# Kernel optimization log

Hardware: AMD Instinct MI355X
Metric: run time of the kernel (lower is better)

Reference implementation:

```python
import jax, jax.numpy as jnp
import numpy as np
from jax import lax


def _conv3x3(x, w, b):
    # x: [b,C,H,W], w: [Cout,Cin,3,3] (OIHW), same padding, stride 1
    y = lax.conv_general_dilated(
        x, w, window_strides=(1, 1), padding='SAME',
        dimension_numbers=('NCHW', 'OIHW', 'NCHW'))
    return y + b[None, :, None, None]


def setup_inputs() -> dict:
    key = jax.random.key(0)
    ks = jax.random.split(key, 8)
    b, C, H, W = 8, 256, 64, 64
    wscale = 0.02  # keep conv outputs O(1) so softmax logits are well-conditioned
    X = jax.random.normal(ks[0], (b, C, H, W), dtype=jnp.float32)
    w1 = jax.random.normal(ks[1], (C, C, 3, 3), dtype=jnp.float32) * wscale
    b1 = jax.random.normal(ks[2], (C,), dtype=jnp.float32) * 0.01
    w2 = jax.random.normal(ks[3], (C, C, 3, 3), dtype=jnp.float32) * wscale
    b2 = jax.random.normal(ks[4], (C,), dtype=jnp.float32) * 0.01
    w3 = jax.random.normal(ks[5], (C, C, 3, 3), dtype=jnp.float32) * wscale
    b3 = jax.random.normal(ks[6], (C,), dtype=jnp.float32) * 0.01
    # alpha_init=0 in the original makes the output identically zero; use a
    # small nonzero alpha so fwd/bwd are non-degenerate for correctness checks.
    alpha = jax.random.normal(ks[7], (), dtype=jnp.float32)
    return {"X": X, "w1": w1, "b1": b1, "w2": w2, "b2": b2,
            "w3": w3, "b3": b3, "alpha": alpha}


def reference(X, w1, b1, w2, b2, w3, b3, alpha):
    b, C, H, W = X.shape
    N = H * W
    A = _conv3x3(X, w1, b1).reshape(b, C, N)  # [b,C,N]
    B = _conv3x3(X, w2, b2).reshape(b, C, N)  # [b,C,N]
    D = _conv3x3(X, w3, b3).reshape(b, C, N)  # [b,C,N]
    # M = softmax(A^T B) over last dim; M: [b,N,N]
    M = jnp.einsum('bcn,bcm->bnm', A, B)
    M = jax.nn.softmax(M, axis=-1)
    # weighted_C = M @ D^T -> [b,N,C]; then to [b,C,H,W]
    out = jnp.einsum('bnm,bcm->bcn', M, D).reshape(b, C, H, W)
    return alpha * out
```

## Files before the change

kernel.cpp:

```cpp
#include <hip/hip_runtime.h>
#include <math.h>

#define BATCH 8
#define CCH   256
#define HH    64
#define WW    64
#define NN    4096

#define BNC   (BATCH * NN * CCH)
#define WELEMS (3 * 8 * 9 * 256 * 32)

typedef __bf16   bf16x8 __attribute__((ext_vector_type(8)));
typedef _Float16 f16x8  __attribute__((ext_vector_type(8)));
typedef _Float16 f16x4  __attribute__((ext_vector_type(4)));
typedef float    f32x4  __attribute__((ext_vector_type(4)));

__global__ void wtrans_kernel(const float* __restrict__ w1,
                              const float* __restrict__ w2,
                              const float* __restrict__ w3,
                              _Float16* __restrict__ Whi,
                              _Float16* __restrict__ Wlo) {
    int e = blockIdx.x * 256 + threadIdx.x;
    int t = e;
    const int ci  = t & 31;  t >>= 5;
    const int co  = t & 255; t >>= 8;
    const int tap = t % 9;   t /= 9;
    const int cc  = t & 7;   t >>= 3;
    const int conv = t;
    const float* src = (conv == 0) ? w1 : (conv == 1) ? w2 : w3;
    const float v = src[co * 2304 + (cc * 32 + ci) * 9 + tap];
    const _Float16 h = (_Float16)v;
    Whi[e] = h;
    Wlo[e] = (_Float16)(v - (float)h);
}

__global__ __launch_bounds__(256)
void xsplit_kernel(const float* __restrict__ X,
                   _Float16* __restrict__ Xhi, _Float16* __restrict__ Xlo) {
    __shared__ float T[64][65];
    const int h = blockIdx.x, c0 = blockIdx.y * 64, bb = blockIdx.z;
    const int t = threadIdx.x;
    const int row = t >> 2, q = (t & 3) * 16;
#pragma unroll
    for (int k = 0; k < 4; ++k) {
        float4 v = *(const float4*)&X[(((size_t)bb * CCH + c0 + row) * HH + h) * WW + q + k * 4];
        *(float4*)&T[row][q + k * 4] = v;
    }
    __syncthreads();
    f16x8 h0, h1, l0, l1;
#pragma unroll
    for (int j = 0; j < 8; ++j) {
        float v = T[q + j][row];
        _Float16 hh = (_Float16)v;
        h0[j] = hh; l0[j] = (_Float16)(v - (float)hh);
    }
#pragma unroll
    for (int j = 0; j < 8; ++j) {
        float v = T[q + 8 + j][row];
        _Float16 hh = (_Float16)v;
        h1[j] = hh; l1[j] = (_Float16)(v - (float)hh);
    }
    const size_t g = (((size_t)bb * HH + h) * WW + row) * CCH + c0 + q;
    *(f16x8*)(Xhi + g) = h0;  *(f16x8*)(Xhi + g + 8) = h1;
    *(f16x8*)(Xlo + g) = l0;  *(f16x8*)(Xlo + g + 8) = l1;
}

__global__ __launch_bounds__(512, 2)
void conv_mfma_kernel(const _Float16* __restrict__ Xhi, const _Float16* __restrict__ Xlo,
                      const _Float16* __restrict__ Whi, const _Float16* __restrict__ Wlo,
                      const float* __restrict__ b1, const float* __restrict__ b2,
                      const float* __restrict__ b3,
                      __bf16* __restrict__ Qhi, __bf16* __restrict__ Qlo,
                      __bf16* __restrict__ Khi, __bf16* __restrict__ Klo,
                      float* __restrict__ Dws) {
    const int h0   = blockIdx.x * 2;
    const int bb   = blockIdx.y;
    const int conv = blockIdx.z;
    const int tid  = threadIdx.x;
    const int wave = tid >> 6;
    const int lane = tid & 63;
    const int quad = lane >> 4;
    const int l16  = lane & 15;
    const int mg   = wave >> 2;
    const int ng   = wave & 3;

    __shared__ _Float16 XsH[4 * 66 * 32];
    __shared__ _Float16 XsL[4 * 66 * 32];

    const bool threePass = (conv < 2);
    const float* bias = (conv == 0) ? b1 : (conv == 1) ? b2 : b3;

    f32x4 acc[4][4];
#pragma unroll
    for (int j = 0; j < 4; ++j) {
        const float bv = bias[ng * 64 + j * 16 + l16];
#pragma unroll
        for (int i = 0; i < 4; ++i) acc[i][j] = (f32x4){bv, bv, bv, bv};
    }

    const f16x8 zf = {0, 0, 0, 0, 0, 0, 0, 0};
    const int xrow = tid >> 7;
    const int xw   = (tid >> 1) & 63;
    const int xch  = (tid & 1) * 16;
    const int xc0  = (tid & 1) * 2;

    if (tid < 256) {
        const int zr = tid >> 6, zc = ((tid >> 5) & 1) ? 65 : 0, zch = tid & 31;
        XsH[(zr * 66 + zc) * 32 + zch] = (_Float16)0;
        XsL[(zr * 66 + zc) * 32 + zch] = (_Float16)0;
    }

    int xb[3];
#pragma unroll
    for (int dw = 0; dw < 3; ++dw)
        xb[dw] = mg * 2112 + (l16 + dw) * 32 + ((quad ^ ((l16 + dw) & 3)) * 8);

    const int wloff = (ng * 64 + l16) * 32 + quad * 8;
    const _Float16* WhB = Whi + (size_t)conv * 589824;
    const _Float16* WlB = Wlo + (size_t)conv * 589824;

    f16x8 wbh[2][4], wbl[2][4];
#pragma unroll
    for (int j = 0; j < 4; ++j) {
        wbh[0][j] = *(const f16x8*)(WhB + wloff + j * 512);
        wbl[0][j] = zf;
        if (threePass) wbl[0][j] = *(const f16x8*)(WlB + wloff + j * 512);
    }

    for (int cc2 = 0; cc2 < 4; ++cc2) {
#pragma unroll
        for (int ccp = 0; ccp < 2; ++ccp) {
            const int cc = cc2 * 2 + ccp;
            __syncthreads();
            {
                const int h = h0 - 1 + xrow;
                f16x8 a0 = zf, a1 = zf, b0 = zf, b1v = zf;
                if ((unsigned)h < (unsigned)HH) {
                    const size_t g = (((size_t)bb * HH + h) * WW + xw) * CCH + cc * 32 + xch;
                    a0 = *(const f16x8*)(Xhi + g);  a1 = *(const f16x8*)(Xhi + g + 8);
                    if (threePass) { b0 = *(const f16x8*)(Xlo + g);  b1v = *(const f16x8*)(Xlo + g + 8); }
                }
                const int col = xw + 1;
                const int lbase = (xrow * 66 + col) * 32;
                const int s3 = col & 3;
                *(f16x8*)&XsH[lbase + ((xc0 ^ s3) * 8)]       = a0;
                *(f16x8*)&XsH[lbase + (((xc0 + 1) ^ s3) * 8)] = a1;
                if (threePass) {
                    *(f16x8*)&XsL[lbase + ((xc0 ^ s3) * 8)]       = b0;
                    *(f16x8*)&XsL[lbase + (((xc0 + 1) ^ s3) * 8)] = b1v;
                }
            }
            __syncthreads();

#pragma unroll
            for (int tap = 0; tap < 9; ++tap) {
                const int p  = (ccp + tap) & 1;
                const int np = p ^ 1;
                {
                    const int nst = cc * 9 + tap + 1;
                    const size_t nb = (size_t)(nst == 72 ? 0 : nst) * 8192 + wloff;
#pragma unroll
                    for (int j = 0; j < 4; ++j) {
                        wbh[np][j] = *(const f16x8*)(WhB + nb + j * 512);
                        if (threePass) wbl[np][j] = *(const f16x8*)(WlB + nb + j * 512);
                    }
                }
                const int dh = tap / 3, dw = tap % 3;
                f16x8 ah[4], al[4];
#pragma unroll
                for (int i = 0; i < 4; ++i) {
                    const int off = xb[dw] + dh * 2112 + i * 512;
                    ah[i] = *(const f16x8*)&XsH[off];
                    if (threePass) al[i] = *(const f16x8*)&XsL[off];
                }
#pragma unroll
                for (int j = 0; j < 4; ++j) {
                    if (threePass) {
#pragma unroll
                        for (int i = 0; i < 4; ++i) {
                            acc[i][j] = __builtin_amdgcn_mfma_f32_16x16x32_f16(ah[i], wbh[p][j], acc[i][j], 0, 0, 0);
                            acc[i][j] = __builtin_amdgcn_mfma_f32_16x16x32_f16(al[i], wbh[p][j], acc[i][j], 0, 0, 0);
                            acc[i][j] = __builtin_amdgcn_mfma_f32_16x16x32_f16(ah[i], wbl[p][j], acc[i][j], 0, 0, 0);
                        }
                    } else {
#pragma unroll
                        for (int i = 0; i < 4; ++i)
                            acc[i][j] = __builtin_amdgcn_mfma_f32_16x16x32_f16(ah[i], wbh[p][j], acc[i][j], 0, 0, 0);
                    }
                }
            }
        }
    }

    const size_t nb = (size_t)bb * NN + (size_t)(h0 + mg) * 64;
    if (threePass) {
        __bf16* Hi = conv ? Khi : Qhi;
        __bf16* Lo = conv ? Klo : Qlo;
#pragma unroll
        for (int i = 0; i < 4; ++i) {
            const int wx0 = i * 16 + quad * 4;
#pragma unroll
            for (int j = 0; j < 4; ++j) {
                const int co = ng * 64 + j * 16 + l16;
#pragma unroll
                for (int r = 0; r < 4; ++r) {
                    const float v = acc[i][j][r];
                    const size_t idx = (nb + wx0 + r) * CCH + co;
                    const __bf16 hq = (__bf16)v;
                    Hi[idx] = hq;
                    Lo[idx] = (__bf16)(v - (float)hq);
                }
            }
        }
    } else {
#pragma unroll
        for (int i = 0; i < 4; ++i) {
            const int wx0 = i * 16 + quad * 4;
#pragma unroll
            for (int j = 0; j < 4; ++j) {
                const int co = ng * 64 + j * 16 + l16;
#pragma unroll
                for (int r = 0; r < 4; ++r)
                    Dws[(nb + wx0 + r) * CCH + co] = acc[i][j][r];
            }
        }
    }
}

__global__ __launch_bounds__(256)
void transpose_v_kernel(const float* __restrict__ D, _Float16* __restrict__ Vt) {
    __shared__ float T[64][65];
    const int n0 = blockIdx.x * 64, c0 = blockIdx.y * 64, bb = blockIdx.z;
    const int t = threadIdx.x;
    const int row = t >> 2, q = (t & 3) * 16;
#pragma unroll
    for (int k = 0; k < 4; ++k) {
        float4 v = *(const float4*)(D + ((size_t)bb * NN + n0 + row) * CCH + c0 + q + k * 4);
        *(float4*)&T[row][q + k * 4] = v;
    }
    __syncthreads();
    f16x8 o0, o1;
#pragma unroll
    for (int j = 0; j < 8; ++j) o0[j] = (_Float16)T[q + j][row];
#pragma unroll
    for (int j = 0; j < 8; ++j) o1[j] = (_Float16)T[q + 8 + j][row];
    _Float16* dst = Vt + ((size_t)bb * CCH + c0 + row) * NN + n0 + q;
    *(f16x8*)dst = o0;
    *(f16x8*)(dst + 8) = o1;
}

__global__ __launch_bounds__(512, 2)
void attn_mfma_kernel(const __bf16* __restrict__ Qhi, const __bf16* __restrict__ Qlo,
                      const __bf16* __restrict__ Khi, const __bf16* __restrict__ Klo,
                      const _Float16* __restrict__ Vt, const float* __restrict__ alpha_p,
                      float* __restrict__ out) {
    const int bb = blockIdx.x & 7;
    const int qb = blockIdx.x >> 3;
    const int n0 = qb * 128;
    const int tid  = threadIdx.x;
    const int wave = tid >> 6;
    const int lane = tid & 63;
    const int quad = lane >> 4;
    const int l16  = lane & 15;
    const int xq   = l16 & 7;

    extern __shared__ __align__(16) unsigned char smem[];
    __bf16*   KsHi = (__bf16*)(smem);
    __bf16*   KsLo = (__bf16*)(smem + 16384);
    _Float16* Vs   = (_Float16*)(smem + 32768);
    _Float16* Pw   = (_Float16*)(smem + 98304) + wave * 16 * 136;

    bf16x8 qh[8], ql[8];
    {
        const size_t base = ((size_t)bb * NN + n0 + wave * 16 + l16) * CCH + quad * 8;
#pragma unroll
        for (int ks = 0; ks < 8; ++ks) {
            qh[ks] = *(const bf16x8*)(Qhi + base + ks * 32);
            ql[ks] = *(const bf16x8*)(Qlo + base + ks * 32);
        }
    }

    f32x4 Oacc[16];
#pragma unroll
    for (int cf = 0; cf < 16; ++cf) Oacc[cf] = (f32x4){0.f, 0.f, 0.f, 0.f};
    float m_i = -INFINITY, l_i = 0.f;

    const int krow = tid >> 2, kq4 = tid & 3;
    const int vrow = tid >> 1, vh = tid & 1;

    bf16x8 kph[2], kpl[2];
    f16x8  vp[4];

    auto kload = [&](int m0_, int cc_) {
#pragma unroll
        for (int i = 0; i < 2; ++i) {
            const int u = kq4 * 2 + i;
            const size_t g = ((size_t)bb * NN + m0_ + krow) * CCH + cc_ * 64 + u * 8;
            kph[i] = *(const bf16x8*)(Khi + g);
            kpl[i] = *(const bf16x8*)(Klo + g);
        }
    };
    auto kwrite = [&]() {
#pragma unroll
        for (int i = 0; i < 2; ++i) {
            const int u = kq4 * 2 + i;
            const int lo = krow * 64 + ((u ^ (krow & 7)) * 8);
            *(bf16x8*)&KsHi[lo] = kph[i];
            *(bf16x8*)&KsLo[lo] = kpl[i];
        }
    };
    auto vload = [&](int m0_, int grp) {
#pragma unroll
        for (int i = 0; i < 4; ++i) {
            const int u = grp * 8 + vh * 4 + i;
            vp[i] = *(const f16x8*)(Vt + ((size_t)bb * CCH + vrow) * NN + m0_ + u * 8);
        }
    };
    auto vwrite = [&](int grp) {
#pragma unroll
        for (int i = 0; i < 4; ++i) {
            const int u = grp * 8 + vh * 4 + i;
            *(f16x8*)&Vs[vrow * 128 + ((u ^ (vrow & 7)) * 8)] = vp[i];
        }
    };

    f32x4 Sacc[8];
    auto schunk = [&](int cc) {
#pragma unroll
        for (int ks = 0; ks < 2; ++ks) {
            const int kq = cc * 2 + ks;
#pragma unroll
            for (int kvt = 0; kvt < 8; ++kvt) {
                const int off = (kvt * 16 + l16) * 64 + (((ks * 4 + quad) ^ xq) * 8);
                const bf16x8 kh = *(const bf16x8*)&KsHi[off];
                const bf16x8 kl = *(const bf16x8*)&KsLo[off];
                Sacc[kvt] = __builtin_amdgcn_mfma_f32_16x16x32_bf16(kh, qh[kq], Sacc[kvt], 0, 0, 0);
                Sacc[kvt] = __builtin_amdgcn_mfma_f32_16x16x32_bf16(kl, qh[kq], Sacc[kvt], 0, 0, 0);
                Sacc[kvt] = __builtin_amdgcn_mfma_f32_16x16x32_bf16(kh, ql[kq], Sacc[kvt], 0, 0, 0);
            }
        }
    };

    kload(0, 0);
    kwrite();
    __syncthreads();

    for (int t = 0; t < 32; ++t) {
        const int m0 = t * 128;
#pragma unroll
        for (int kvt = 0; kvt < 8; ++kvt) Sacc[kvt] = (f32x4){0.f, 0.f, 0.f, 0.f};

        for (int cc = 0; cc < 3; ++cc) {
            kload(m0, cc + 1);
            schunk(cc);
            __syncthreads();
            kwrite();
            __syncthreads();
        }

        vload(m0, 0);
        schunk(3);
        vwrite(0);
        vload(m0, 1);

        float mx = -INFINITY;
#pragma unroll
        for (int kvt = 0; kvt < 8; ++kvt)
#pragma unroll
            for (int r = 0; r < 4; ++r) mx = fmaxf(mx, Sacc[kvt][r]);
        mx = fmaxf(mx, __shfl_xor(mx, 16, 64));
        mx = fmaxf(mx, __shfl_xor(mx, 32, 64));
        const float mnew = fmaxf(m_i, mx);
        float rs = 0.f;
#pragma unroll
        for (int kvt = 0; kvt < 8; ++kvt) {
            f16x4 pw;
#pragma unroll
            for (int r = 0; r < 4; ++r) {
                const float p = __expf(Sacc[kvt][r] - mnew);
                rs += p;
                pw[r] = (_Float16)p;
            }
            *(f16x4*)&Pw[l16 * 136 + kvt * 16 + quad * 4] = pw;
        }
        rs += __shfl_xor(rs, 16, 64);
        rs += __shfl_xor(rs, 32, 64);
        const float scale = __expf(m_i - mnew);
        l_i = l_i * scale + rs;
        m_i = mnew;
#pragma unroll
        for (int cf = 0; cf < 16; ++cf) {
            Oacc[cf][0] *= scale;
            Oacc[cf][1] *= scale;
            Oacc[cf][2] *= scale;
            Oacc[cf][3] *= scale;
        }
        vwrite(1);
        __syncthreads();

        kload((t == 31) ? 0 : m0 + 128, 0);
        f16x8 pf[4];
#pragma unroll
        for (int kvf = 0; kvf < 4; ++kvf)
            pf[kvf] = *(const f16x8*)&Pw[l16 * 136 + kvf * 32 + quad * 8];
#pragma unroll
        for (int cf = 0; cf < 16; ++cf) {
#pragma unroll
            for (int kvf = 0; kvf < 4; ++kvf) {
                const f16x8 vf = *(const f16x8*)&Vs[(cf * 16 + l16) * 128 + (((kvf * 4 + quad) ^ xq) * 8)];
                Oacc[cf] = __builtin_amdgcn_mfma_f32_16x16x32_f16(vf, pf[kvf], Oacc[cf], 0, 0, 0);
            }
        }
        kwrite();
        __syncthreads();
    }

    const float alpha = *alpha_p;
    const float inv = alpha / l_i;
    const int qg = n0 + wave * 16 + l16;
#pragma unroll
    for (int cf = 0; cf < 16; ++cf) {
#pragma unroll
        for (int r = 0; r < 4; ++r) {
            const int c = cf * 16 + quad * 4 + r;
            out[((size_t)bb * CCH + c) * NN + qg] = Oacc[cf][r] * inv;
        }
    }
}

extern "C" void kernel_launch(void* const* d_in, const int* in_sizes, int n_in,
                              void* d_out, int out_size, void* d_ws, size_t ws_size,
                              hipStream_t stream) {
    const float* X  = (const float*)d_in[0];
    const float* w1 = (const float*)d_in[1];
    const float* b1 = (const float*)d_in[2];
    const float* w2 = (const float*)d_in[3];
    const float* b2 = (const float*)d_in[4];
    const float* w3 = (const float*)d_in[5];
    const float* b3 = (const float*)d_in[6];
    const float* alpha = (const float*)d_in[7];
    float* out = (float*)d_out;

    float*    Dws = (float*)d_ws;
    __bf16*   Qhi = (__bf16*)(Dws + (size_t)BNC);
    __bf16*   Qlo = Qhi + (size_t)BNC;
    __bf16*   Khi = Qlo + (size_t)BNC;
    __bf16*   Klo = Khi + (size_t)BNC;
    _Float16* Vt  = (_Float16*)(Klo + (size_t)BNC);
    _Float16* Xhi = Vt + (size_t)BNC;
    _Float16* Xlo = Xhi + (size_t)BNC;
    _Float16* Whi = Xlo + (size_t)BNC;
    _Float16* Wlo = Whi + (size_t)WELEMS;

    wtrans_kernel<<<dim3(WELEMS / 256), 256, 0, stream>>>(w1, w2, w3, Whi, Wlo);

    xsplit_kernel<<<dim3(HH, CCH / 64, BATCH), 256, 0, stream>>>(X, Xhi, Xlo);

    conv_mfma_kernel<<<dim3(HH / 2, BATCH, 3), 512, 0, stream>>>(
        Xhi, Xlo, Whi, Wlo, b1, b2, b3, Qhi, Qlo, Khi, Klo, Dws);

    transpose_v_kernel<<<dim3(NN / 64, CCH / 64, BATCH), 256, 0, stream>>>(Dws, Vt);

    attn_mfma_kernel<<<dim3(256), 512, 133120, stream>>>(
        Qhi, Qlo, Khi, Klo, Vt, alpha, out);
}
```

Measured before the change: 586.2 us.

## Split PV GEMM by channel per wave, loading V directly into registers

The PV product is repartitioned. Each wave now owns 32 output channels for all 128 queries instead of 16 queries for all 256 channels, and reads its V fragments straight from global memory into registers instead of staging V through shared memory. K staging becomes double-buffered, so each chunk needs one barrier instead of two. P tiles and the per-row rescale factors and final normalisers are shared through LDS, which shrinks the LDS footprint. The cost is uncoalesced-ish direct global V loads, extra LDS reads of P for all query tiles, and a different output store pattern.

```diff
diff --git a/kernel.cpp b/kernel.cpp
--- a/kernel.cpp
+++ b/kernel.cpp
@@ -265,10 +265,10 @@
     const int xq   = l16 & 7;
 
     extern __shared__ __align__(16) unsigned char smem[];
-    __bf16*   KsHi = (__bf16*)(smem);
-    __bf16*   KsLo = (__bf16*)(smem + 16384);
-    _Float16* Vs   = (_Float16*)(smem + 32768);
-    _Float16* Pw   = (_Float16*)(smem + 98304) + wave * 16 * 136;
+    _Float16* PwA  = (_Float16*)(smem + 65536);
+    float*    Ssc  = (float*)(smem + 100352);
+    float*    Linv = (float*)(smem + 100864);
+    _Float16* Pw   = PwA + wave * (16 * 136);
 
     bf16x8 qh[8], ql[8];
     {
@@ -280,16 +280,16 @@
         }
     }
 
-    f32x4 Oacc[16];
-#pragma unroll
-    for (int cf = 0; cf < 16; ++cf) Oacc[cf] = (f32x4){0.f, 0.f, 0.f, 0.f};
+    f32x4 Oacc[2][8];
+#pragma unroll
+    for (int cf = 0; cf < 2; ++cf)
+#pragma unroll
+        for (int qt = 0; qt < 8; ++qt) Oacc[cf][qt] = (f32x4){0.f, 0.f, 0.f, 0.f};
     float m_i = -INFINITY, l_i = 0.f;
 
     const int krow = tid >> 2, kq4 = tid & 3;
-    const int vrow = tid >> 1, vh = tid & 1;
 
     bf16x8 kph[2], kpl[2];
-    f16x8  vp[4];
 
     auto kload = [&](int m0_, int cc_) {
 #pragma unroll
@@ -300,40 +300,26 @@
             kpl[i] = *(const bf16x8*)(Klo + g);
         }
     };
-    auto kwrite = [&]() {
+    auto kwrite = [&](__bf16* H, __bf16* L) {
 #pragma unroll
         for (int i = 0; i < 2; ++i) {
             const int u = kq4 * 2 + i;
             const int lo = krow * 64 + ((u ^ (krow & 7)) * 8);
-            *(bf16x8*)&KsHi[lo] = kph[i];
-            *(bf16x8*)&KsLo[lo] = kpl[i];
+            *(bf16x8*)&H[lo] = kph[i];
+            *(bf16x8*)&L[lo] = kpl[i];
         }
     };
-    auto vload = [&](int m0_, int grp) {
-#pragma unroll
-        for (int i = 0; i < 4; ++i) {
-            const int u = grp * 8 + vh * 4 + i;
-            vp[i] = *(const f16x8*)(Vt + ((size_t)bb * CCH + vrow) * NN + m0_ + u * 8);
-        }
-    };
-    auto vwrite = [&](int grp) {
-#pragma unroll
-        for (int i = 0; i < 4; ++i) {
-            const int u = grp * 8 + vh * 4 + i;
-            *(f16x8*)&Vs[vrow * 128 + ((u ^ (vrow & 7)) * 8)] = vp[i];
-        }
-    };
 
     f32x4 Sacc[8];
-    auto schunk = [&](int cc) {
+    auto schunk = [&](int cc, const __bf16* KH, const __bf16* KL) {
 #pragma unroll
         for (int ks = 0; ks < 2; ++ks) {
             const int kq = cc * 2 + ks;
 #pragma unroll
             for (int kvt = 0; kvt < 8; ++kvt) {
                 const int off = (kvt * 16 + l16) * 64 + (((ks * 4 + quad) ^ xq) * 8);
-                const bf16x8 kh = *(const bf16x8*)&KsHi[off];
-                const bf16x8 kl = *(const bf16x8*)&KsLo[off];
+                const bf16x8 kh = *(const bf16x8*)&KH[off];
+                const bf16x8 kl = *(const bf16x8*)&KL[off];
                 Sacc[kvt] = __builtin_amdgcn_mfma_f32_16x16x32_bf16(kh, qh[kq], Sacc[kvt], 0, 0, 0);
                 Sacc[kvt] = __builtin_amdgcn_mfma_f32_16x16x32_bf16(kl, qh[kq], Sacc[kvt], 0, 0, 0);
                 Sacc[kvt] = __builtin_amdgcn_mfma_f32_16x16x32_bf16(kh, ql[kq], Sacc[kvt], 0, 0, 0);
@@ -342,7 +328,7 @@
     };
 
     kload(0, 0);
-    kwrite();
+    kwrite((__bf16*)smem, (__bf16*)(smem + 16384));
     __syncthreads();
 
     for (int t = 0; t < 32; ++t) {
@@ -350,18 +336,27 @@
 #pragma unroll
         for (int kvt = 0; kvt < 8; ++kvt) Sacc[kvt] = (f32x4){0.f, 0.f, 0.f, 0.f};
 
-        for (int cc = 0; cc < 3; ++cc) {
-            kload(m0, cc + 1);
-            schunk(cc);
+#pragma unroll
+        for (int cc = 0; cc < 4; ++cc) {
+            const int p = cc & 1;
+            const __bf16* KH = (const __bf16*)(smem + p * 32768);
+            const __bf16* KL = (const __bf16*)(smem + p * 32768 + 16384);
+            __bf16* WH = (__bf16*)(smem + (p ^ 1) * 32768);
+            __bf16* WL = (__bf16*)(smem + (p ^ 1) * 32768 + 16384);
+            kload(cc < 3 ? m0 : ((t == 31) ? 0 : m0 + 128), (cc + 1) & 3);
+            schunk(cc, KH, KL);
+            kwrite(WH, WL);
             __syncthreads();
-            kwrite();
-            __syncthreads();
-        }
-
-        vload(m0, 0);
-        schunk(3);
-        vwrite(0);
-        vload(m0, 1);
+        }
+
+        f16x8 vf[2][4];
+#pragma unroll
+        for (int cf = 0; cf < 2; ++cf)
+#pragma unroll
+            for (int kvf = 0; kvf < 4; ++kvf)
+                vf[cf][kvf] = *(const f16x8*)(Vt +
+                    ((size_t)bb * CCH + wave * 32 + cf * 16 + l16) * NN +
+                    m0 + kvf * 32 + quad * 8);
 
         float mx = -INFINITY;
 #pragma unroll
@@ -386,45 +381,53 @@
         rs += __shfl_xor(rs, 16, 64);
         rs += __shfl_xor(rs, 32, 64);
         const float scale = __expf(m_i - mnew);
+        if (quad == 0) Ssc[wave * 16 + l16] = scale;
         l_i = l_i * scale + rs;
         m_i = mnew;
-#pragma unroll
-        for (int cf = 0; cf < 16; ++cf) {
-            Oacc[cf][0] *= scale;
-            Oacc[cf][1] *= scale;
-            Oacc[cf][2] *= scale;
-            Oacc[cf][3] *= scale;
-        }
-        vwrite(1);
         __syncthreads();
 
-        kload((t == 31) ? 0 : m0 + 128, 0);
-        f16x8 pf[4];
-#pragma unroll
-        for (int kvf = 0; kvf < 4; ++kvf)
-            pf[kvf] = *(const f16x8*)&Pw[l16 * 136 + kvf * 32 + quad * 8];
-#pragma unroll
-        for (int cf = 0; cf < 16; ++cf) {
-#pragma unroll
-            for (int kvf = 0; kvf < 4; ++kvf) {
-                const f16x8 vf = *(const f16x8*)&Vs[(cf * 16 + l16) * 128 + (((kvf * 4 + quad) ^ xq) * 8)];
-                Oacc[cf] = __builtin_amdgcn_mfma_f32_16x16x32_f16(vf, pf[kvf], Oacc[cf], 0, 0, 0);
-            }
-        }
-        kwrite();
+        float sc[8];
+#pragma unroll
+        for (int qt = 0; qt < 8; ++qt) sc[qt] = Ssc[qt * 16 + l16];
+#pragma unroll
+        for (int cf = 0; cf < 2; ++cf)
+#pragma unroll
+            for (int qt = 0; qt < 8; ++qt) {
+                Oacc[cf][qt][0] *= sc[qt];
+                Oacc[cf][qt][1] *= sc[qt];
+                Oacc[cf][qt][2] *= sc[qt];
+                Oacc[cf][qt][3] *= sc[qt];
+            }
+
+#pragma unroll
+        for (int qt = 0; qt < 8; ++qt) {
+            const _Float16* Pq = PwA + qt * (16 * 136);
+            f16x8 pf[4];
+#pragma unroll
+            for (int kvf = 0; kvf < 4; ++kvf)
+                pf[kvf] = *(const f16x8*)&Pq[l16 * 136 + kvf * 32 + quad * 8];
+#pragma unroll
+            for (int cf = 0; cf < 2; ++cf)
+#pragma unroll
+                for (int kvf = 0; kvf < 4; ++kvf)
+                    Oacc[cf][qt] = __builtin_amdgcn_mfma_f32_16x16x32_f16(vf[cf][kvf], pf[kvf], Oacc[cf][qt], 0, 0, 0);
+        }
         __syncthreads();
     }
 
     const float alpha = *alpha_p;
-    const float inv = alpha / l_i;
-    const int qg = n0 + wave * 16 + l16;
-#pragma unroll
-    for (int cf = 0; cf < 16; ++cf) {
-#pragma unroll
-        for (int r = 0; r < 4; ++r) {
-            const int c = cf * 16 + quad * 4 + r;
-            out[((size_t)bb * CCH + c) * NN + qg] = Oacc[cf][r] * inv;
-        }
+    if (quad == 0) Linv[wave * 16 + l16] = alpha / l_i;
+    __syncthreads();
+#pragma unroll
+    for (int qt = 0; qt < 8; ++qt) {
+        const float inv = Linv[qt * 16 + l16];
+#pragma unroll
+        for (int cf = 0; cf < 2; ++cf)
+#pragma unroll
+            for (int r = 0; r < 4; ++r) {
+                const int c = wave * 32 + cf * 16 + quad * 4 + r;
+                out[((size_t)bb * CCH + c) * NN + n0 + qt * 16 + l16] = Oacc[cf][qt][r] * inv;
+            }
     }
 }
 
@@ -461,6 +464,6 @@
 
     transpose_v_kernel<<<dim3(NN / 64, CCH / 64, BATCH), 256, 0, stream>>>(Dws, Vt);
 
-    attn_mfma_kernel<<<dim3(256), 512, 133120, stream>>>(
+    attn_mfma_kernel<<<dim3(256), 512, 101376, stream>>>(
         Qhi, Qlo, Khi, Klo, Vt, alpha, out);
 }
```

Result: no change. 591.8 us (+1.0%).
